# Kernel tuning notes

Hardware: AMD Instinct MI355X
Metric: run time of the kernel (lower is better)

The kernel has to match this reference:

```python
import jax, jax.numpy as jnp
import numpy as np
from jax import lax

# program token ids
PAD, START, END, SCENE, INTERSECT, FILT, RELATE, QUERY = range(8)
SKIP = (PAD, START, END)


def conv2d(x, w, b, dil=1):
    # 'same' padding for odd kernels (3x3 pad=dil, 1x1 pad=0), NCHW/OIHW
    pad = dil * (w.shape[2] // 2)
    y = lax.conv_general_dilated(x, w, (1, 1), [(pad, pad), (pad, pad)],
                                 rhs_dilation=(dil, dil),
                                 dimension_numbers=('NCHW', 'OIHW', 'NCHW'))
    return y + b[None, :, None, None]


def maxpool2(x):
    return lax.reduce_window(x, -jnp.inf, lax.max, (1, 1, 2, 2), (1, 1, 2, 2), 'VALID')


def exec_program(prog, feat_input, p):
    """Run one (concrete) program over a batch of stem features. prog: tuple of ints,
    executed in reversed order exactly like TbDNet.forward."""
    B, _, H, W = feat_input.shape
    output = feat_input
    saved = None
    for t in reversed(prog):
        if t in SKIP:
            continue
        if t == SCENE:
            saved = output
            output = jnp.ones((B, 1, H, W), feat_input.dtype)
        elif t == INTERSECT:  # AndModule: elementwise min of attentions
            output = jnp.minimum(output, saved)
        elif t == FILT:
            a = feat_input * output  # [B,D,H,W] * [B,1,H,W]
            a = jax.nn.relu(conv2d(a, p['att_w1'], p['att_b1']))
            a = jax.nn.relu(conv2d(a, p['att_w2'], p['att_b2']))
            output = jax.nn.sigmoid(conv2d(a, p['att_w3'], p['att_b3']))
        elif t == RELATE:  # RelateModule: dilated conv stack (1,2,4,8,1) -> conv1x1 sigmoid
            a = feat_input * output
            for w, b, d in ((p['rel_w1'], p['rel_b1'], 1), (p['rel_w2'], p['rel_b2'], 2),
                            (p['rel_w3'], p['rel_b3'], 4), (p['rel_w4'], p['rel_b4'], 8),
                            (p['rel_w5'], p['rel_b5'], 1)):
                a = jax.nn.relu(conv2d(a, w, b, d))
            output = jax.nn.sigmoid(conv2d(a, p['rel_w6'], p['rel_b6']))
        elif t == QUERY:
            a = feat_input * output
            a = jax.nn.relu(conv2d(a, p['qry_w1'], p['qry_b1']))
            output = jax.nn.relu(conv2d(a, p['qry_w2'], p['qry_b2']))
    return output


def tbd_forward(feats, programs_np, p):
    B = feats.shape[0]
    stem = jax.nn.relu(conv2d(feats, p['stem_w1'], p['stem_b1']))
    stem = jax.nn.relu(conv2d(stem, p['stem_w2'], p['stem_b2']))  # [B,D,H,W]
    D, H, W = stem.shape[1], stem.shape[2], stem.shape[3]
    # group samples by identical program so dispatch runs batched, not per-sample
    groups = {}
    for n in range(B):
        groups.setdefault(tuple(int(v) for v in programs_np[n]), []).append(n)
    mod_out = jnp.zeros((B, D, H, W), feats.dtype)
    for prog, idxs in groups.items():
        idx = jnp.array(idxs)
        mod_out = mod_out.at[idx].set(exec_program(prog, stem[idx], p))
    # classifier: conv1x1 -> relu -> maxpool2 -> flatten -> fc -> relu -> fc
    x = jax.nn.relu(conv2d(mod_out, p['cls_w'], p['cls_b']))
    x = maxpool2(x)                        # [B,1024,7,7]
    x = x.reshape(B, -1)                   # [B,50176]
    x = jax.nn.relu(x @ p['fc1_w'].T + p['fc1_b'])
    return x @ p['fc2_w'].T + p['fc2_b']   # [B,28]


def setup_inputs() -> dict:
    key = jax.random.key(0)
    ks = iter(jax.random.split(key, 64))
    def rn(shape, s=0.05):
        return jax.random.normal(next(ks), shape, dtype=jnp.float32) * s
    B, Cin, H, W, D, P, L, A = 64, 1024, 14, 14, 128, 1024, 1024, 28
    feats = jax.random.normal(next(ks), (B, Cin, H, W), dtype=jnp.float32)
    # stored programs; execution order is reversed(stored)
    progA = [START, QUERY, FILT, RELATE, FILT, SCENE, END, PAD]            # scene->filter->relate->filter->query
    progB = [START, QUERY, INTERSECT, FILT, SCENE, FILT, SCENE, END]       # two filter branches -> intersect -> query
    programs = jnp.array([progA] * (B // 2) + [progB] * (B // 2), dtype=jnp.int32)
    inp = {'feats': feats, 'programs': programs,
           'stem_w1': rn((D, Cin, 3, 3), 0.02), 'stem_b1': rn((D,)),
           'stem_w2': rn((D, D, 3, 3)), 'stem_b2': rn((D,)),
           'att_w1': rn((D, D, 3, 3)), 'att_b1': rn((D,)),
           'att_w2': rn((D, D, 3, 3)), 'att_b2': rn((D,)),
           'att_w3': rn((1, D, 1, 1)), 'att_b3': rn((1,)),
           'rel_w1': rn((D, D, 3, 3)), 'rel_b1': rn((D,)),
           'rel_w2': rn((D, D, 3, 3)), 'rel_b2': rn((D,)),
           'rel_w3': rn((D, D, 3, 3)), 'rel_b3': rn((D,)),
           'rel_w4': rn((D, D, 3, 3)), 'rel_b4': rn((D,)),
           'rel_w5': rn((D, D, 3, 3)), 'rel_b5': rn((D,)),
           'rel_w6': rn((1, D, 1, 1)), 'rel_b6': rn((1,)),
           'qry_w1': rn((D, D, 3, 3)), 'qry_b1': rn((D,)),
           'qry_w2': rn((D, D, 3, 3)), 'qry_b2': rn((D,)),
           'cls_w': rn((P, D, 1, 1)), 'cls_b': rn((P,)),
           'fc1_w': rn((L, P * (H // 2) * (W // 2)), 0.01), 'fc1_b': rn((L,)),
           'fc2_w': rn((A, L)), 'fc2_b': rn((A,))}
    return inp


PARAM_NAMES = ['stem_w1', 'stem_b1', 'stem_w2', 'stem_b2',
               'att_w1', 'att_b1', 'att_w2', 'att_b2', 'att_w3', 'att_b3',
               'rel_w1', 'rel_b1', 'rel_w2', 'rel_b2', 'rel_w3', 'rel_b3',
               'rel_w4', 'rel_b4', 'rel_w5', 'rel_b5', 'rel_w6', 'rel_b6',
               'qry_w1', 'qry_b1', 'qry_w2', 'qry_b2',
               'cls_w', 'cls_b', 'fc1_w', 'fc1_b', 'fc2_w', 'fc2_b']


def reference(feats, programs, stem_w1, stem_b1, stem_w2, stem_b2,
              att_w1, att_b1, att_w2, att_b2, att_w3, att_b3,
              rel_w1, rel_b1, rel_w2, rel_b2, rel_w3, rel_b3,
              rel_w4, rel_b4, rel_w5, rel_b5, rel_w6, rel_b6,
              qry_w1, qry_b1, qry_w2, qry_b2,
              cls_w, cls_b, fc1_w, fc1_b, fc2_w, fc2_b):
    vals = [stem_w1, stem_b1, stem_w2, stem_b2,
            att_w1, att_b1, att_w2, att_b2, att_w3, att_b3,
            rel_w1, rel_b1, rel_w2, rel_b2, rel_w3, rel_b3,
            rel_w4, rel_b4, rel_w5, rel_b5, rel_w6, rel_b6,
            qry_w1, qry_b1, qry_w2, qry_b2,
            cls_w, cls_b, fc1_w, fc1_b, fc2_w, fc2_b]
    p = dict(zip(PARAM_NAMES, vals))
    return tbd_forward(feats, np.asarray(programs), p)
```

## Files before the change

### kernel.cpp

```cpp
#include <hip/hip_runtime.h>
#include <math.h>


typedef __attribute__((ext_vector_type(8)))  short   short8;
typedef __attribute__((ext_vector_type(8)))  __bf16  bf16x8;
typedef __attribute__((ext_vector_type(4)))  float   f32x4;

#define NROUNDS 12
#define NKS 98

#define B_WSTEM1 0UL
#define B_WSTEM2 2359296UL
#define B_WMOD   2654208UL
#define B_WCLS   5308416UL
#define B_STEM   5570560UL
#define B_XA     8781824UL
#define B_XB     11993088UL
#define B_FEAT   15204352UL
#define B_ATTN   18415616UL
#define B_SAVED  18465792UL
#define B_SCHED  18515968UL
#define B_ACTB   18520064UL
#define B_FC1T   24942592UL
#define B_P1X1   25204736UL
#define B_S1P    67108864UL
#define B_FC1P   100663296UL

__device__ __forceinline__ unsigned short f2bf(float f) {
    unsigned int b = __float_as_uint(f);
    b += 0x7fffu + ((b >> 16) & 1u);
    return (unsigned short)(b >> 16);
}
__device__ __forceinline__ float bf2f(unsigned short u) {
    return __uint_as_float(((unsigned int)u) << 16);
}
__device__ __forceinline__ f32x4 mfma16(bf16x8 a, bf16x8 b, f32x4 c) {
    return __builtin_amdgcn_mfma_f32_16x16x32_bf16(a, b, c, 0, 0, 0);
}

struct RepackArgs { const float* src[12]; };

__global__ __launch_bounds__(256) void k_repack(RepackArgs a, char* ws)
{
    const int y = blockIdx.y;
    const float* __restrict__ src = a.src[y];
    int gid = blockIdx.x * 256 + threadIdx.x;
    int gsz = gridDim.x * 256;
    if (y == 11) {
        unsigned short* dst = (unsigned short*)(ws + B_WCLS);
        for (int i = gid; i < 131072; i += gsz) dst[i] = f2bf(src[i]);
    } else {
        const int IC = (y == 0) ? 1024 : 128;
        const int lg = (y == 0) ? 10 : 7;
        unsigned short* dst = (unsigned short*)(ws + ((y == 0) ? B_WSTEM1
                                    : (y == 1) ? B_WSTEM2
                                    : B_WMOD + (size_t)(y - 2) * 294912));
        const int total = 9 << (lg + 7);
        for (int i = gid; i < total; i += gsz) {
            int ic = i & (IC - 1);
            int oc = (i >> lg) & 127;
            int t  = i >> (lg + 7);
            dst[i] = f2bf(src[((size_t)oc * IC + ic) * 9 + t]);
        }
    }
}

__global__ __launch_bounds__(256) void k_decode_init(const int* __restrict__ prog, char* ws)
{
    int gid = blockIdx.x * 256 + threadIdx.x;
    int gsz = gridDim.x * 256;
    float* attn  = (float*)(ws + B_ATTN);
    float* saved = (float*)(ws + B_SAVED);
    float* p1    = (float*)(ws + B_P1X1);
    for (int i = gid; i < 64 * 196; i += gsz) { attn[i] = 1.0f; saved[i] = 1.0f; }
    for (int i = gid; i < 8 * 64 * 196; i += gsz) p1[i] = 0.0f;
    unsigned int* fz = (unsigned int*)(ws + B_FEAT);
    for (int i = gid; i < 64 * 25088 / 2; i += gsz) fz[i] = 0u;
    if (gid < 64) {
        int n = gid;
        int ent[NROUNDS];
        for (int r = 0; r < NROUNDS; ++r) ent[r] = 0;
        int rc = 0, nslot = 0;
        int pscene = 0, pinter = 0, pmat = 0, pmw = 0;
#define PREBITS ((pscene<<17)|(pinter<<18)|(pmat<<19)|(pmw<<22))
#define CLRPRE  (pscene = pinter = pmat = pmw = 0)
#define EMIT(v) do { if (rc < NROUNDS) ent[rc++] = (v); } while (0)
        for (int j = 7; j >= 0; --j) {
            int t = prog[n * 8 + j];
            switch (t) {
                case 3: pscene = 1; break;
                case 4: pinter = 1; break;
                case 5: {
                    int e1 = 3 | (0<<4) | (1<<8) | (1<<12) | (2<<13) | (0<<15) | PREBITS;
                    CLRPRE; EMIT(e1);
                    int e2 = 3 | (1<<4) | (1<<8) | (0<<12) | (0<<13) | (1<<15)
                               | (1<<23) | (0<<24) | (nslot<<25);
                    EMIT(e2);
                    pmat = nslot + 1; pmw = 0; nslot++;
                    break;
                }
                case 6: {
                    int e1 = 3 | (2<<4) | (1<<8) | (1<<12) | (2<<13) | (0<<15) | PREBITS;
                    CLRPRE; EMIT(e1);
                    EMIT(3 | (3<<4) | (2<<8) | (0<<12) | (0<<13) | (1<<15));
                    EMIT(3 | (4<<4) | (4<<8) | (0<<12) | (1<<13) | (0<<15));
                    EMIT(3 | (5<<4) | (8<<8) | (0<<12) | (0<<13) | (1<<15));
                    EMIT(3 | (6<<4) | (1<<8) | (0<<12) | (1<<13) | (0<<15)
                           | (1<<23) | (1<<24) | (nslot<<25));
                    pmat = nslot + 1; pmw = 1; nslot++;
                    break;
                }
                case 7: {
                    int e1 = 3 | (7<<4) | (1<<8) | (1<<12) | (2<<13) | (0<<15) | PREBITS;
                    CLRPRE; EMIT(e1);
                    EMIT(3 | (8<<4) | (1<<8) | (0<<12) | (0<<13) | (2<<15));
                    break;
                }
                default: break;
            }
        }
#undef EMIT
#undef PREBITS
#undef CLRPRE
        int* sched = (int*)(ws + B_SCHED);
        for (int r = 0; r < NROUNDS; ++r) sched[n * NROUNDS + r] = ent[r];
    }
}

__global__ __launch_bounds__(512) void k_stem1p(const float* __restrict__ feats,
                                                const unsigned short* __restrict__ wrep,
                                                char* ws)
{
    __shared__ unsigned short s_img[197 * 136];
    const int bx = blockIdx.x;
    const int n = bx >> 3, ks = bx & 7;
    const int tid = threadIdx.x, lane = tid & 63;
    const int w = tid >> 6, wm = w & 1, wn = w >> 1;
    const int l15 = lane & 15, lq = lane >> 4;

    if (tid < 68) ((unsigned int*)s_img)[196 * 68 + tid] = 0u;

    int pglob[4], pbyt[4], pyv[4], pxv[4];
#pragma unroll
    for (int j = 0; j < 4; ++j) {
        int p  = (wn + 4 * j) * 16 + l15;
        pglob[j] = p;
        int py = p / 14;
        pyv[j] = (p < 196) ? py : 10000;
        pxv[j] = p - py * 14;
        pbyt[j] = p * 272 + lq * 16;
    }
    const int zaddr = 196 * 272 + lq * 16;
    const int nJ = (wn == 0) ? 4 : 3;

    f32x4 acc[4][4];
#pragma unroll
    for (int m = 0; m < 4; ++m)
#pragma unroll
        for (int j = 0; j < 4; ++j) acc[m][j] = (f32x4){0.f, 0.f, 0.f, 0.f};

    const int icg = tid & 31;
    const int qq0 = tid >> 5;
    const int icb = ks * 128;

    const float* sf = feats + ((size_t)n * 1024 + icb) * 196;
    for (int qq = qq0; qq < 49; qq += 16) {
        const float* p0 = sf + icg * 4 * 196 + qq * 4;
        float4 r0 = *(const float4*)(p0);
        float4 r1 = *(const float4*)(p0 + 196);
        float4 r2 = *(const float4*)(p0 + 392);
        float4 r3 = *(const float4*)(p0 + 588);
#pragma unroll
        for (int e = 0; e < 4; ++e) {
            uint2 v;
            v.x = (unsigned int)f2bf(((const float*)&r0)[e]) |
                  ((unsigned int)f2bf(((const float*)&r1)[e]) << 16);
            v.y = (unsigned int)f2bf(((const float*)&r2)[e]) |
                  ((unsigned int)f2bf(((const float*)&r3)[e]) << 16);
            *(uint2*)(s_img + (qq * 4 + e) * 136 + icg * 4) = v;
        }
    }
    __syncthreads();

#pragma unroll
    for (int t = 0; t < 9; ++t) {
        const int dy = t / 3 - 1, dx = t % 3 - 1;
        int baddr[4];
#pragma unroll
        for (int j = 0; j < 4; ++j) {
            int yy = pyv[j] + dy, xx = pxv[j] + dx;
            bool ok = ((unsigned)yy < 14u) && ((unsigned)xx < 14u);
            baddr[j] = ok ? (pbyt[j] + (dy * 14 + dx) * 272) : zaddr;
        }
#pragma unroll
        for (int kc = 0; kc < 4; ++kc) {
            const unsigned short* wt = wrep +
                ((size_t)(t * 128 + wm * 64 + l15) * 1024 + icb + kc * 32 + lq * 8);
            bf16x8 am[4];
#pragma unroll
            for (int m = 0; m < 4; ++m)
                am[m] = *(const bf16x8*)(wt + (size_t)m * 16 * 1024);
#pragma unroll
            for (int j = 0; j < 4; ++j) {
                if (j < nJ) {
                    bf16x8 b = *(const bf16x8*)((const char*)s_img + baddr[j] + kc * 64);
#pragma unroll
                    for (int m = 0; m < 4; ++m)
                        acc[m][j] = mfma16(am[m], b, acc[m][j]);
                }
            }
        }
    }

    unsigned short* part = (unsigned short*)(ws + B_S1P);
#pragma unroll
    for (int m = 0; m < 4; ++m) {
        const int oc = wm * 64 + m * 16 + lq * 4;
#pragma unroll
        for (int j = 0; j < 4; ++j) {
            if (j < nJ) {
                int p = pglob[j];
                if (p < 196) {
                    unsigned int lo = (unsigned int)f2bf(acc[m][j][0]) |
                                      ((unsigned int)f2bf(acc[m][j][1]) << 16);
                    unsigned int hi = (unsigned int)f2bf(acc[m][j][2]) |
                                      ((unsigned int)f2bf(acc[m][j][3]) << 16);
                    uint2 pk; pk.x = lo; pk.y = hi;
                    *(uint2*)(part + (((size_t)ks * 64 + n) * 196 + p) * 128 + oc) = pk;
                }
            }
        }
    }
}

__global__ __launch_bounds__(256) void k_stem1r(const char* __restrict__ ws_c,
                                                const float* __restrict__ bias,
                                                unsigned short* __restrict__ xa)
{
    int i = blockIdx.x * 256 + threadIdx.x;
    const unsigned short* part = (const unsigned short*)(ws_c + B_S1P);
    int oc8 = (i & 15) * 8;
    int np  = i >> 4;
    float s[8] = {};
#pragma unroll
    for (int ks = 0; ks < 8; ++ks) {
        short8 v = *(const short8*)(part + (((size_t)ks * 64) * 196 + np) * 128 + oc8);
#pragma unroll
        for (int e = 0; e < 8; ++e) s[e] += bf2f((unsigned short)v[e]);
    }
    short8 o;
#pragma unroll
    for (int e = 0; e < 8; ++e)
        o[e] = (short)f2bf(fmaxf(s[e] + bias[oc8 + e], 0.f));
    *(short8*)(xa + (size_t)np * 128 + oc8) = o;
}

__device__ void conv_core32(const unsigned short* __restrict__ srcB,
                            const float* __restrict__ s_gate,
                            const unsigned short* __restrict__ wrep,
                            const float* __restrict__ bias,
                            unsigned short* __restrict__ dst,
                            int dil, int oct, int pxh,
                            unsigned short* s_img,
                            int post, const float* __restrict__ pwv,
                            float* __restrict__ pdst)
{
    const int tid  = threadIdx.x, lane = tid & 63;
    const int w    = tid >> 6, wm = w & 1, wn = w >> 1;
    const int l15  = lane & 15, lq = lane >> 4;

    if (tid < 68) ((unsigned int*)s_img)[196 * 68 + tid] = 0u;

    int pglob[4], pbyt[4], pyv[4], pxv[4];
#pragma unroll
    for (int j = 0; j < 4; ++j) {
        int nt = wn + 2 * j;
        int p  = (pxh * 7 + nt) * 16 + l15;
        pglob[j] = p;
        int py = p / 14;
        pyv[j] = (p < 196) ? py : 10000;
        pxv[j] = p - py * 14;
        pbyt[j] = p * 272 + lq * 16;
    }
    const int zaddr = 196 * 272 + lq * 16;
    const int nNT = (wn == 0) ? 4 : 3;

    f32x4 acc[4];
#pragma unroll
    for (int j = 0; j < 4; ++j) acc[j] = (f32x4){0.f, 0.f, 0.f, 0.f};

    if (s_gate) {
        for (int i = tid; i < 196 * 16; i += 256) {
            int p = i >> 4, c8 = (i & 15) * 8;
            short8 v = *(const short8*)(srcB + p * 128 + c8);
            float g = s_gate[p];
            short8 ov;
#pragma unroll
            for (int e = 0; e < 8; ++e)
                ov[e] = (short)f2bf(bf2f((unsigned short)v[e]) * g);
            *(short8*)(s_img + p * 136 + c8) = ov;
        }
    } else {
        for (int i = tid; i < 196 * 16; i += 256) {
            int p = i >> 4, c8 = (i & 15) * 8;
            *(short8*)(s_img + p * 136 + c8) = *(const short8*)(srcB + p * 128 + c8);
        }
    }
    __syncthreads();

    const unsigned short* wlane = wrep + (size_t)(oct * 32 + wm * 16 + l15) * 128 + lq * 8;
#pragma unroll
    for (int t = 0; t < 9; ++t) {
        const int dy = (t / 3 - 1) * dil, dx = (t % 3 - 1) * dil;
        int baddr[4];
#pragma unroll
        for (int j = 0; j < 4; ++j) {
            int yy = pyv[j] + dy, xx = pxv[j] + dx;
            bool ok = ((unsigned)yy < 14u) && ((unsigned)xx < 14u);
            baddr[j] = ok ? (pbyt[j] + (dy * 14 + dx) * 272) : zaddr;
        }
        const unsigned short* wt = wlane + (size_t)(t * 128) * 128;
#pragma unroll
        for (int kc = 0; kc < 4; ++kc) {
            bf16x8 a0 = *(const bf16x8*)(wt + kc * 32);
#pragma unroll
            for (int j = 0; j < 4; ++j) {
                if (j < nNT) {
                    bf16x8 b = *(const bf16x8*)((const char*)s_img + baddr[j] + kc * 64);
                    acc[j] = mfma16(a0, b, acc[j]);
                }
            }
        }
    }

    const int oc = oct * 32 + wm * 16 + lq * 4;
    const float4 b4 = *(const float4*)(bias + oc);
    float4 wv4;
    if (post) wv4 = *(const float4*)(pwv + oc);
#pragma unroll
    for (int j = 0; j < 4; ++j) {
        if (j < nNT) {
            int p = pglob[j];
            if (p < 196) {
                float v0 = fmaxf(acc[j][0] + b4.x, 0.f);
                float v1 = fmaxf(acc[j][1] + b4.y, 0.f);
                float v2 = fmaxf(acc[j][2] + b4.z, 0.f);
                float v3 = fmaxf(acc[j][3] + b4.w, 0.f);
                uint2 pk;
                pk.x = (unsigned int)f2bf(v0) | ((unsigned int)f2bf(v1) << 16);
                pk.y = (unsigned int)f2bf(v2) | ((unsigned int)f2bf(v3) << 16);
                *(uint2*)(dst + p * 128 + oc) = pk;
                if (post) {
                    float s = v0 * wv4.x + v1 * wv4.y + v2 * wv4.z + v3 * wv4.w;
                    atomicAdd(pdst + p, s);
                }
            }
        }
    }
}

__global__ __launch_bounds__(256) void k_conv_stem2(const unsigned short* __restrict__ srcBall,
                                                    const unsigned short* __restrict__ wrep,
                                                    const float* __restrict__ bias,
                                                    unsigned short* __restrict__ dstall)
{
    __shared__ unsigned short s_img[197 * 136];
    const int n = blockIdx.x >> 3, oct = (blockIdx.x >> 1) & 3, pxh = blockIdx.x & 1;
    conv_core32(srcBall + (size_t)n * 25088, nullptr, wrep, bias,
                dstall + (size_t)n * 25088, 1, oct, pxh, s_img, 0, nullptr, nullptr);
}

struct RArgs {
    char* ws;
    const float* mbias[9];
    const float* w1x1[2];
    const float* b1x1[2];
};

__global__ __launch_bounds__(256) void k_round(RArgs a, int r)
{
    __shared__ unsigned short s_img[197 * 136];
    __shared__ float s_gate[196];
    const int bx = blockIdx.x;
    const int n = bx >> 3, oct = (bx >> 1) & 3, pxh = bx & 1;
    char* ws = a.ws;
    const int* sched = (const int*)(ws + B_SCHED);
    const int e = sched[n * NROUNDS + r];
    if ((e & 15) == 0) return;
    const int tid = threadIdx.x;
    const int wset = (e >> 4) & 15, dil = (e >> 8) & 15, gatef = (e >> 12) & 1;
    const int srcid = (e >> 13) & 3, dstid = (e >> 15) & 3;
    const int fscene = (e >> 17) & 1, finter = (e >> 18) & 1;
    const int mslot = (e >> 19) & 7, mw = (e >> 22) & 1;
    const int post = (e >> 23) & 1, pw = (e >> 24) & 1, pslot = (e >> 25) & 7;

    float* attn  = (float*)(ws + B_ATTN)  + n * 196;
    float* saved = (float*)(ws + B_SAVED) + n * 196;
    float* p1    = (float*)(ws + B_P1X1);

    if (gatef) {
        if (tid < 196) {
            float cur = attn[tid];
            if (mslot) {
                float pv = p1[(size_t)(mslot - 1) * 12544 + n * 196 + tid];
                cur = 1.0f / (1.0f + __expf(-(pv + a.b1x1[mw][0])));
            }
            if (fscene) { saved[tid] = cur; cur = 1.0f; }
            if (finter) { cur = fminf(cur, saved[tid]); }
            if (mslot | fscene | finter) attn[tid] = cur;
            s_gate[tid] = cur;
        }
        __syncthreads();
    }

    const unsigned short* src = (const unsigned short*)(ws +
            (srcid == 2 ? B_STEM : srcid == 1 ? B_XB : B_XA)) + (size_t)n * 25088;
    unsigned short* dst = (unsigned short*)(ws +
            (dstid == 2 ? B_FEAT : dstid == 1 ? B_XB : B_XA)) + (size_t)n * 25088;
    const unsigned short* wrep = (const unsigned short*)(ws + B_WMOD) + (size_t)wset * 9 * 128 * 128;

    conv_core32(src, gatef ? s_gate : nullptr, wrep, a.mbias[wset], dst,
                dil, oct, pxh, s_img,
                post, post ? a.w1x1[pw] : nullptr,
                post ? (p1 + (size_t)pslot * 12544 + n * 196) : nullptr);
}

__global__ __launch_bounds__(256) void k_cls_pool(const unsigned short* __restrict__ featall,
                                                  const unsigned short* __restrict__ clsw,
                                                  const float* __restrict__ clsb,
                                                  unsigned short* __restrict__ actB)
{
    __shared__ char smem[197 * 272 + 64 * 200 * 4];
    unsigned short* s_img = (unsigned short*)smem;
    float* s_pool = (float*)(smem + 197 * 272);
    const int n = blockIdx.x >> 4, pt = blockIdx.x & 15;
    const int tid = threadIdx.x, lane = tid & 63, w = tid >> 6;
    const int l15 = lane & 15, lq = lane >> 4;
    const unsigned short* feat = featall + (size_t)n * 25088;

    if (tid < 68) ((unsigned int*)s_img)[196 * 68 + tid] = 0u;
    for (int i = tid; i < 196 * 16; i += 256) {
        int p = i >> 4, c8 = (i & 15) * 8;
        *(short8*)(s_img + p * 136 + c8) = *(const short8*)(feat + p * 128 + c8);
    }
    f32x4 acc[14];
#pragma unroll
    for (int j = 0; j < 14; ++j) acc[j] = (f32x4){0.f, 0.f, 0.f, 0.f};
    __syncthreads();

    const unsigned short* wl = clsw + (size_t)(pt * 64 + w * 16 + l15) * 128 + lq * 8;
#pragma unroll
    for (int kc = 0; kc < 4; ++kc) {
        bf16x8 a0 = *(const bf16x8*)(wl + kc * 32);
#pragma unroll
        for (int j = 0; j < 14; ++j) {
            int p = j * 16 + l15;
            int ba = (p < 196) ? (p * 272 + lq * 16 + kc * 64) : (196 * 272 + lq * 16);
            bf16x8 b = *(const bf16x8*)((const char*)s_img + ba);
            acc[j] = mfma16(a0, b, acc[j]);
        }
    }
    const int oc = pt * 64 + w * 16 + lq * 4;
    const float4 b4 = *(const float4*)(clsb + oc);
    const int pl = w * 16 + lq * 4;
#pragma unroll
    for (int j = 0; j < 14; ++j) {
        int p = j * 16 + l15;
        if (p < 196) {
            s_pool[(pl + 0) * 200 + p] = fmaxf(acc[j][0] + b4.x, 0.f);
            s_pool[(pl + 1) * 200 + p] = fmaxf(acc[j][1] + b4.y, 0.f);
            s_pool[(pl + 2) * 200 + p] = fmaxf(acc[j][2] + b4.z, 0.f);
            s_pool[(pl + 3) * 200 + p] = fmaxf(acc[j][3] + b4.w, 0.f);
        }
    }
    __syncthreads();
    for (int i = tid; i < 64 * 49; i += 256) {
        int plx = i / 49, q = i - plx * 49;
        int py = q / 7, qx = q - py * 7;
        const float* rp = s_pool + plx * 200 + py * 28 + qx * 2;
        float m = fmaxf(fmaxf(rp[0], rp[1]), fmaxf(rp[14], rp[15]));
        int k = (pt * 64 + plx) * 49 + q;
        int kb = k >> 6, lq2 = (k >> 4) & 3, hi = (k >> 3) & 1, e = k & 7;
        actB[((((size_t)kb * 4 + lq2) * 2 + hi) * 64 + n) * 8 + e] = f2bf(m);
    }
}

__global__ __launch_bounds__(256) void k_fc1p(const unsigned short* __restrict__ actB,
                                              const float* __restrict__ w,
                                              float* __restrict__ part)
{
    __shared__ unsigned short s_w[64 * 264];
    const int jt = blockIdx.x & 15, ks = blockIdx.x >> 4;
    const int tid = threadIdx.x, lane = tid & 63, wv = tid >> 6;
    const int l15 = lane & 15, lq = lane >> 4;
    const int k0 = ks * 512;
    const int r4 = tid & 3, l4 = (tid >> 2) & 15, rw = tid >> 6;

    f32x4 acc[4];
#pragma unroll
    for (int t = 0; t < 4; ++t) acc[t] = (f32x4){0.f, 0.f, 0.f, 0.f};

    float4 pf[4][4];

#define FC1_LOAD(ss_) do {                                                        \
    _Pragma("unroll")                                                             \
    for (int pass = 0; pass < 4; ++pass) {                                        \
        const int row_ = pass * 16 + rw * 4 + r4;                                 \
        const float* wp_ = w + (size_t)(jt * 64 + row_) * 50176 + k0              \
                             + (ss_) * 256 + l4 * 16;                             \
        pf[pass][0] = *(const float4*)(wp_);                                      \
        pf[pass][1] = *(const float4*)(wp_ + 4);                                  \
        pf[pass][2] = *(const float4*)(wp_ + 8);                                  \
        pf[pass][3] = *(const float4*)(wp_ + 12);                                 \
    } } while (0)

    FC1_LOAD(0);

    for (int ss = 0; ss < 2; ++ss) {
        __syncthreads();
#pragma unroll
        for (int pass = 0; pass < 4; ++pass) {
            const int row = pass * 16 + rw * 4 + r4;
            bf16x8 c0, c1;
            c0[0] = (__bf16)pf[pass][0].x; c0[1] = (__bf16)pf[pass][0].y;
            c0[2] = (__bf16)pf[pass][0].z; c0[3] = (__bf16)pf[pass][0].w;
            c0[4] = (__bf16)pf[pass][1].x; c0[5] = (__bf16)pf[pass][1].y;
            c0[6] = (__bf16)pf[pass][1].z; c0[7] = (__bf16)pf[pass][1].w;
            c1[0] = (__bf16)pf[pass][2].x; c1[1] = (__bf16)pf[pass][2].y;
            c1[2] = (__bf16)pf[pass][2].z; c1[3] = (__bf16)pf[pass][2].w;
            c1[4] = (__bf16)pf[pass][3].x; c1[5] = (__bf16)pf[pass][3].y;
            c1[6] = (__bf16)pf[pass][3].z; c1[7] = (__bf16)pf[pass][3].w;
            *(bf16x8*)(s_w + row * 264 + l4 * 16)     = c0;
            *(bf16x8*)(s_w + row * 264 + l4 * 16 + 8) = c1;
        }
        __syncthreads();
        if (ss < 1) FC1_LOAD(1);

        const unsigned short* arow = s_w + (wv * 16 + l15) * 264;
#pragma unroll
        for (int kk = 0; kk < 8; ++kk) {
            bf16x8 a = *(const bf16x8*)(arow + kk * 32 + lq * 8);
            const int kglob = k0 + ss * 256 + kk * 32 + lq * 8;
            const int kb = kglob >> 6, lq2 = (kglob >> 4) & 3, hi = (kglob >> 3) & 1;
            const unsigned short* bp = actB +
                ((((size_t)kb * 4 + lq2) * 2 + hi) * 64 + l15) * 8;
#pragma unroll
            for (int t = 0; t < 4; ++t) {
                bf16x8 b = *(const bf16x8*)(bp + t * 128);
                acc[t] = mfma16(a, b, acc[t]);
            }
        }
    }
#undef FC1_LOAD

    float* pbase = part + ((size_t)ks * 1024 + jt * 64 + wv * 16 + lq * 4) * 64 + l15;
#pragma unroll
    for (int t = 0; t < 4; ++t)
#pragma unroll
        for (int r = 0; r < 4; ++r)
            pbase[(size_t)r * 64 + t * 16] = acc[t][r];
}

__global__ __launch_bounds__(256) void k_fc1r(const float* __restrict__ part,
                                              const float* __restrict__ b,
                                              float* __restrict__ fc1T)
{
    int i = blockIdx.x * 256 + threadIdx.x;
    if (i >= 65536) return;
    float s = 0.0f;
    for (int ks = 0; ks < NKS; ++ks) s += part[(size_t)ks * 65536 + i];
    int j = i >> 6;
    fc1T[i] = fmaxf(s + b[j], 0.0f);
}

__global__ __launch_bounds__(256) void k_fc2(const float* __restrict__ fc1T,
                                             const float* __restrict__ w,
                                             const float* __restrict__ b,
                                             float* __restrict__ out)
{
    __shared__ float red[256];
    const int a_ = blockIdx.x;
    const int tid = threadIdx.x, lane = tid & 63, q = tid >> 6;
    float acc = 0.0f;
    const float* wr = w + (size_t)a_ * 1024;
    for (int k = q * 256; k < q * 256 + 256; ++k)
        acc = fmaf(fc1T[k * 64 + lane], wr[k], acc);
    red[tid] = acc;
    __syncthreads();
    if (q == 0) {
        float s = red[tid] + red[tid + 64] + red[tid + 128] + red[tid + 192] + b[a_];
        out[lane * 28 + a_] = s;
    }
}

extern "C" void kernel_launch(void* const* d_in, const int* in_sizes, int n_in,
                              void* d_out, int out_size, void* d_ws, size_t ws_size,
                              hipStream_t stream)
{
    const float* feats = (const float*)d_in[0];
    const int*   prog  = (const int*)d_in[1];
    char* ws  = (char*)d_ws;
    float* out = (float*)d_out;

    RepackArgs ra;
    ra.src[0]  = (const float*)d_in[2];
    ra.src[1]  = (const float*)d_in[4];
    ra.src[2]  = (const float*)d_in[6];
    ra.src[3]  = (const float*)d_in[8];
    ra.src[4]  = (const float*)d_in[12];
    ra.src[5]  = (const float*)d_in[14];
    ra.src[6]  = (const float*)d_in[16];
    ra.src[7]  = (const float*)d_in[18];
    ra.src[8]  = (const float*)d_in[20];
    ra.src[9]  = (const float*)d_in[24];
    ra.src[10] = (const float*)d_in[26];
    ra.src[11] = (const float*)d_in[28];

    k_repack<<<dim3(64, 12), 256, 0, stream>>>(ra, ws);
    k_decode_init<<<256, 256, 0, stream>>>(prog, ws);

    k_stem1p<<<512, 512, 0, stream>>>(feats, (const unsigned short*)(ws + B_WSTEM1), ws);
    k_stem1r<<<784, 256, 0, stream>>>(ws, (const float*)d_in[3],
                                      (unsigned short*)(ws + B_XA));

    k_conv_stem2<<<512, 256, 0, stream>>>((const unsigned short*)(ws + B_XA),
                                          (const unsigned short*)(ws + B_WSTEM2),
                                          (const float*)d_in[5],
                                          (unsigned short*)(ws + B_STEM));

    RArgs ga;
    ga.ws = ws;
    ga.mbias[0] = (const float*)d_in[7];
    ga.mbias[1] = (const float*)d_in[9];
    ga.mbias[2] = (const float*)d_in[13];
    ga.mbias[3] = (const float*)d_in[15];
    ga.mbias[4] = (const float*)d_in[17];
    ga.mbias[5] = (const float*)d_in[19];
    ga.mbias[6] = (const float*)d_in[21];
    ga.mbias[7] = (const float*)d_in[25];
    ga.mbias[8] = (const float*)d_in[27];
    ga.w1x1[0]  = (const float*)d_in[10];
    ga.w1x1[1]  = (const float*)d_in[22];
    ga.b1x1[0]  = (const float*)d_in[11];
    ga.b1x1[1]  = (const float*)d_in[23];

    for (int r = 0; r < NROUNDS; ++r)
        k_round<<<512, 256, 0, stream>>>(ga, r);

    k_cls_pool<<<1024, 256, 0, stream>>>((const unsigned short*)(ws + B_FEAT),
                                         (const unsigned short*)(ws + B_WCLS),
                                         (const float*)d_in[29],
                                         (unsigned short*)(ws + B_ACTB));
    k_fc1p<<<1568, 256, 0, stream>>>((const unsigned short*)(ws + B_ACTB),
                                     (const float*)d_in[30], (float*)(ws + B_FC1P));
    k_fc1r<<<256, 256, 0, stream>>>((const float*)(ws + B_FC1P), (const float*)d_in[31],
                                    (float*)(ws + B_FC1T));
    k_fc2<<<28, 256, 0, stream>>>((const float*)(ws + B_FC1T), (const float*)d_in[32],
                                  (const float*)d_in[33], out);
}
```

Baseline: 525.9 us.

## Fuse round launches into a persistent cooperative kernel with grid syncs

Merges the stem reduce, stem conv2 and every program round into one cooperative persistent kernel of 256 blocks by 512 threads, with grid.sync between stages. Each block now handles a full image and output-channel tile instead of half the pixels. The repack and decode/init kernels are folded into one launch, and fc1-reduce plus fc2 become a single cooperative kernel. The goal is to remove many launch gaps and the per-round schedule decode overhead, at the cost of grid-wide barriers, half the block count and larger blocks. NROUNDS drops from 12 to 11, which shrinks the schedule.

Result: slower. 785.6 us (+49.4%).

```diff
diff --git a/kernel.cpp b/kernel.cpp
--- a/kernel.cpp
+++ b/kernel.cpp
@@ -1,12 +1,15 @@
 #include <hip/hip_runtime.h>
+#include <hip/hip_cooperative_groups.h>
 #include <math.h>
+
+namespace cg = cooperative_groups;
 
 
 typedef __attribute__((ext_vector_type(8)))  short   short8;
 typedef __attribute__((ext_vector_type(8)))  __bf16  bf16x8;
 typedef __attribute__((ext_vector_type(4)))  float   f32x4;
 
-#define NROUNDS 12
+#define NROUNDS 11
 #define NKS 98
 
 #define B_WSTEM1 0UL
@@ -38,37 +41,38 @@
     return __builtin_amdgcn_mfma_f32_16x16x32_bf16(a, b, c, 0, 0, 0);
 }
 
-struct RepackArgs { const float* src[12]; };
-
-__global__ __launch_bounds__(256) void k_repack(RepackArgs a, char* ws)
-{
-    const int y = blockIdx.y;
-    const float* __restrict__ src = a.src[y];
-    int gid = blockIdx.x * 256 + threadIdx.x;
-    int gsz = gridDim.x * 256;
-    if (y == 11) {
-        unsigned short* dst = (unsigned short*)(ws + B_WCLS);
-        for (int i = gid; i < 131072; i += gsz) dst[i] = f2bf(src[i]);
-    } else {
-        const int IC = (y == 0) ? 1024 : 128;
-        const int lg = (y == 0) ? 10 : 7;
-        unsigned short* dst = (unsigned short*)(ws + ((y == 0) ? B_WSTEM1
-                                    : (y == 1) ? B_WSTEM2
-                                    : B_WMOD + (size_t)(y - 2) * 294912));
-        const int total = 9 << (lg + 7);
-        for (int i = gid; i < total; i += gsz) {
-            int ic = i & (IC - 1);
-            int oc = (i >> lg) & 127;
-            int t  = i >> (lg + 7);
-            dst[i] = f2bf(src[((size_t)oc * IC + ic) * 9 + t]);
-        }
-    }
-}
-
-__global__ __launch_bounds__(256) void k_decode_init(const int* __restrict__ prog, char* ws)
-{
-    int gid = blockIdx.x * 256 + threadIdx.x;
-    int gsz = gridDim.x * 256;
+struct PrepArgs { const float* src[12]; const int* prog; char* ws; };
+
+__global__ __launch_bounds__(256) void k_prep(PrepArgs a)
+{
+    char* ws = a.ws;
+    const int bx = blockIdx.x;
+    if (bx < 768) {
+        const int y = bx >> 6;
+        const float* __restrict__ src = a.src[y];
+        int gid = (bx & 63) * 256 + threadIdx.x;
+        int gsz = 64 * 256;
+        if (y == 11) {
+            unsigned short* dst = (unsigned short*)(ws + B_WCLS);
+            for (int i = gid; i < 131072; i += gsz) dst[i] = f2bf(src[i]);
+        } else {
+            const int IC = (y == 0) ? 1024 : 128;
+            const int lg = (y == 0) ? 10 : 7;
+            unsigned short* dst = (unsigned short*)(ws + ((y == 0) ? B_WSTEM1
+                                        : (y == 1) ? B_WSTEM2
+                                        : B_WMOD + (size_t)(y - 2) * 294912));
+            const int total = 9 << (lg + 7);
+            for (int i = gid; i < total; i += gsz) {
+                int ic = i & (IC - 1);
+                int oc = (i >> lg) & 127;
+                int t  = i >> (lg + 7);
+                dst[i] = f2bf(src[((size_t)oc * IC + ic) * 9 + t]);
+            }
+        }
+        return;
+    }
+    int gid = (bx - 768) * 256 + threadIdx.x;
+    int gsz = 256 * 256;
     float* attn  = (float*)(ws + B_ATTN);
     float* saved = (float*)(ws + B_SAVED);
     float* p1    = (float*)(ws + B_P1X1);
@@ -78,6 +82,7 @@
     for (int i = gid; i < 64 * 25088 / 2; i += gsz) fz[i] = 0u;
     if (gid < 64) {
         int n = gid;
+        const int* prog = a.prog;
         int ent[NROUNDS];
         for (int r = 0; r < NROUNDS; ++r) ent[r] = 0;
         int rc = 0, nslot = 0;
@@ -93,9 +98,8 @@
                 case 5: {
                     int e1 = 3 | (0<<4) | (1<<8) | (1<<12) | (2<<13) | (0<<15) | PREBITS;
                     CLRPRE; EMIT(e1);
-                    int e2 = 3 | (1<<4) | (1<<8) | (0<<12) | (0<<13) | (1<<15)
-                               | (1<<23) | (0<<24) | (nslot<<25);
-                    EMIT(e2);
+                    EMIT(3 | (1<<4) | (1<<8) | (0<<12) | (0<<13) | (1<<15)
+                           | (1<<23) | (0<<24) | (nslot<<25));
                     pmat = nslot + 1; pmw = 0; nslot++;
                     break;
                 }
@@ -233,49 +237,45 @@
     }
 }
 
-__global__ __launch_bounds__(256) void k_stem1r(const char* __restrict__ ws_c,
-                                                const float* __restrict__ bias,
-                                                unsigned short* __restrict__ xa)
-{
-    int i = blockIdx.x * 256 + threadIdx.x;
-    const unsigned short* part = (const unsigned short*)(ws_c + B_S1P);
-    int oc8 = (i & 15) * 8;
-    int np  = i >> 4;
-    float s[8] = {};
-#pragma unroll
-    for (int ks = 0; ks < 8; ++ks) {
-        short8 v = *(const short8*)(part + (((size_t)ks * 64) * 196 + np) * 128 + oc8);
-#pragma unroll
-        for (int e = 0; e < 8; ++e) s[e] += bf2f((unsigned short)v[e]);
-    }
-    short8 o;
-#pragma unroll
-    for (int e = 0; e < 8; ++e)
-        o[e] = (short)f2bf(fmaxf(s[e] + bias[oc8 + e], 0.f));
-    *(short8*)(xa + (size_t)np * 128 + oc8) = o;
-}
-
-__device__ void conv_core32(const unsigned short* __restrict__ srcB,
-                            const float* __restrict__ s_gate,
-                            const unsigned short* __restrict__ wrep,
-                            const float* __restrict__ bias,
-                            unsigned short* __restrict__ dst,
-                            int dil, int oct, int pxh,
-                            unsigned short* s_img,
-                            int post, const float* __restrict__ pwv,
-                            float* __restrict__ pdst)
-{
-    const int tid  = threadIdx.x, lane = tid & 63;
-    const int w    = tid >> 6, wm = w & 1, wn = w >> 1;
-    const int l15  = lane & 15, lq = lane >> 4;
+__device__ void conv512(const unsigned short* __restrict__ src,
+                        const float* __restrict__ s_gate,
+                        const unsigned short* __restrict__ wrep,
+                        const float* __restrict__ bias,
+                        unsigned short* __restrict__ dst,
+                        int dil, int oct,
+                        unsigned short* s_img,
+                        int post, const float* __restrict__ pwv,
+                        float* __restrict__ pdst)
+{
+    const int tid = threadIdx.x, lane = tid & 63;
+    const int w = tid >> 6, wm = w & 1, wn = w >> 1;
+    const int l15 = lane & 15, lq = lane >> 4;
 
     if (tid < 68) ((unsigned int*)s_img)[196 * 68 + tid] = 0u;
 
+    if (s_gate) {
+        for (int i = tid; i < 196 * 16; i += 512) {
+            int p = i >> 4, c8 = (i & 15) * 8;
+            short8 v = *(const short8*)(src + p * 128 + c8);
+            float g = s_gate[p];
+            short8 ov;
+#pragma unroll
+            for (int e = 0; e < 8; ++e)
+                ov[e] = (short)f2bf(bf2f((unsigned short)v[e]) * g);
+            *(short8*)(s_img + p * 136 + c8) = ov;
+        }
+    } else {
+        for (int i = tid; i < 196 * 16; i += 512) {
+            int p = i >> 4, c8 = (i & 15) * 8;
+            *(short8*)(s_img + p * 136 + c8) = *(const short8*)(src + p * 128 + c8);
+        }
+    }
+    __syncthreads();
+
     int pglob[4], pbyt[4], pyv[4], pxv[4];
 #pragma unroll
     for (int j = 0; j < 4; ++j) {
-        int nt = wn + 2 * j;
-        int p  = (pxh * 7 + nt) * 16 + l15;
+        int p  = (wn + 4 * j) * 16 + l15;
         pglob[j] = p;
         int py = p / 14;
         pyv[j] = (p < 196) ? py : 10000;
@@ -283,30 +283,11 @@
         pbyt[j] = p * 272 + lq * 16;
     }
     const int zaddr = 196 * 272 + lq * 16;
-    const int nNT = (wn == 0) ? 4 : 3;
+    const int nJ = (wn == 0) ? 4 : 3;
 
     f32x4 acc[4];
 #pragma unroll
     for (int j = 0; j < 4; ++j) acc[j] = (f32x4){0.f, 0.f, 0.f, 0.f};
-
-    if (s_gate) {
-        for (int i = tid; i < 196 * 16; i += 256) {
-            int p = i >> 4, c8 = (i & 15) * 8;
-            short8 v = *(const short8*)(srcB + p * 128 + c8);
-            float g = s_gate[p];
-            short8 ov;
-#pragma unroll
-            for (int e = 0; e < 8; ++e)
-                ov[e] = (short)f2bf(bf2f((unsigned short)v[e]) * g);
-            *(short8*)(s_img + p * 136 + c8) = ov;
-        }
-    } else {
-        for (int i = tid; i < 196 * 16; i += 256) {
-            int p = i >> 4, c8 = (i & 15) * 8;
-            *(short8*)(s_img + p * 136 + c8) = *(const short8*)(srcB + p * 128 + c8);
-        }
-    }
-    __syncthreads();
 
     const unsigned short* wlane = wrep + (size_t)(oct * 32 + wm * 16 + l15) * 128 + lq * 8;
 #pragma unroll
@@ -325,7 +306,7 @@
             bf16x8 a0 = *(const bf16x8*)(wt + kc * 32);
 #pragma unroll
             for (int j = 0; j < 4; ++j) {
-                if (j < nNT) {
+                if (j < nJ) {
                     bf16x8 b = *(const bf16x8*)((const char*)s_img + baddr[j] + kc * 64);
                     acc[j] = mfma16(a0, b, acc[j]);
                 }
@@ -339,7 +320,7 @@
     if (post) wv4 = *(const float4*)(pwv + oc);
 #pragma unroll
     for (int j = 0; j < 4; ++j) {
-        if (j < nNT) {
+        if (j < nJ) {
             int p = pglob[j];
             if (p < 196) {
                 float v0 = fmaxf(acc[j][0] + b4.x, 0.f);
@@ -359,70 +340,95 @@
     }
 }
 
-__global__ __launch_bounds__(256) void k_conv_stem2(const unsigned short* __restrict__ srcBall,
-                                                    const unsigned short* __restrict__ wrep,
-                                                    const float* __restrict__ bias,
-                                                    unsigned short* __restrict__ dstall)
-{
-    __shared__ unsigned short s_img[197 * 136];
-    const int n = blockIdx.x >> 3, oct = (blockIdx.x >> 1) & 3, pxh = blockIdx.x & 1;
-    conv_core32(srcBall + (size_t)n * 25088, nullptr, wrep, bias,
-                dstall + (size_t)n * 25088, 1, oct, pxh, s_img, 0, nullptr, nullptr);
-}
-
-struct RArgs {
+struct IArgs {
     char* ws;
+    const float* stem1b;
+    const float* stem2b;
     const float* mbias[9];
     const float* w1x1[2];
     const float* b1x1[2];
 };
 
-__global__ __launch_bounds__(256) void k_round(RArgs a, int r)
+__global__ __launch_bounds__(512) void k_interp(IArgs a)
 {
     __shared__ unsigned short s_img[197 * 136];
     __shared__ float s_gate[196];
+    cg::grid_group grid = cg::this_grid();
+    char* ws = a.ws;
     const int bx = blockIdx.x;
-    const int n = bx >> 3, oct = (bx >> 1) & 3, pxh = bx & 1;
-    char* ws = a.ws;
+    const int n = bx >> 2, oct = bx & 3;
+    const int tid = threadIdx.x;
+
+    {
+        const unsigned short* part = (const unsigned short*)(ws + B_S1P);
+        unsigned short* xa = (unsigned short*)(ws + B_XA);
+        for (int i = bx * 512 + tid; i < 64 * 196 * 16; i += 256 * 512) {
+            int oc8 = (i & 15) * 8;
+            int np  = i >> 4;
+            float s[8] = {};
+#pragma unroll
+            for (int ks = 0; ks < 8; ++ks) {
+                short8 v = *(const short8*)(part + (((size_t)ks * 64) * 196 + np) * 128 + oc8);
+#pragma unroll
+                for (int e = 0; e < 8; ++e) s[e] += bf2f((unsigned short)v[e]);
+            }
+            short8 o;
+#pragma unroll
+            for (int e = 0; e < 8; ++e)
+                o[e] = (short)f2bf(fmaxf(s[e] + a.stem1b[oc8 + e], 0.f));
+            *(short8*)(xa + (size_t)np * 128 + oc8) = o;
+        }
+    }
+    grid.sync();
+
+    conv512((const unsigned short*)(ws + B_XA) + (size_t)n * 25088, nullptr,
+            (const unsigned short*)(ws + B_WSTEM2), a.stem2b,
+            (unsigned short*)(ws + B_STEM) + (size_t)n * 25088,
+            1, oct, s_img, 0, nullptr, nullptr);
+    grid.sync();
+
     const int* sched = (const int*)(ws + B_SCHED);
-    const int e = sched[n * NROUNDS + r];
-    if ((e & 15) == 0) return;
-    const int tid = threadIdx.x;
-    const int wset = (e >> 4) & 15, dil = (e >> 8) & 15, gatef = (e >> 12) & 1;
-    const int srcid = (e >> 13) & 3, dstid = (e >> 15) & 3;
-    const int fscene = (e >> 17) & 1, finter = (e >> 18) & 1;
-    const int mslot = (e >> 19) & 7, mw = (e >> 22) & 1;
-    const int post = (e >> 23) & 1, pw = (e >> 24) & 1, pslot = (e >> 25) & 7;
-
     float* attn  = (float*)(ws + B_ATTN)  + n * 196;
     float* saved = (float*)(ws + B_SAVED) + n * 196;
     float* p1    = (float*)(ws + B_P1X1);
 
-    if (gatef) {
-        if (tid < 196) {
-            float cur = attn[tid];
-            if (mslot) {
-                float pv = p1[(size_t)(mslot - 1) * 12544 + n * 196 + tid];
-                cur = 1.0f / (1.0f + __expf(-(pv + a.b1x1[mw][0])));
-            }
-            if (fscene) { saved[tid] = cur; cur = 1.0f; }
-            if (finter) { cur = fminf(cur, saved[tid]); }
-            if (mslot | fscene | finter) attn[tid] = cur;
-            s_gate[tid] = cur;
-        }
-        __syncthreads();
-    }
-
-    const unsigned short* src = (const unsigned short*)(ws +
-            (srcid == 2 ? B_STEM : srcid == 1 ? B_XB : B_XA)) + (size_t)n * 25088;
-    unsigned short* dst = (unsigned short*)(ws +
-            (dstid == 2 ? B_FEAT : dstid == 1 ? B_XB : B_XA)) + (size_t)n * 25088;
-    const unsigned short* wrep = (const unsigned short*)(ws + B_WMOD) + (size_t)wset * 9 * 128 * 128;
-
-    conv_core32(src, gatef ? s_gate : nullptr, wrep, a.mbias[wset], dst,
-                dil, oct, pxh, s_img,
-                post, post ? a.w1x1[pw] : nullptr,
-                post ? (p1 + (size_t)pslot * 12544 + n * 196) : nullptr);
+    for (int r = 0; r < NROUNDS; ++r) {
+        const int e = sched[n * NROUNDS + r];
+        if (e & 15) {
+            const int wset = (e >> 4) & 15, dil = (e >> 8) & 15, gatef = (e >> 12) & 1;
+            const int srcid = (e >> 13) & 3, dstid = (e >> 15) & 3;
+            const int fscene = (e >> 17) & 1, finter = (e >> 18) & 1;
+            const int mslot = (e >> 19) & 7, mw = (e >> 22) & 1;
+            const int post = (e >> 23) & 1, pw = (e >> 24) & 1, pslot = (e >> 25) & 7;
+
+            if (gatef) {
+                if (tid < 196) {
+                    float cur = attn[tid];
+                    if (mslot) {
+                        float pv = p1[(size_t)(mslot - 1) * 12544 + n * 196 + tid];
+                        cur = 1.0f / (1.0f + __expf(-(pv + a.b1x1[mw][0])));
+                    }
+                    if (fscene) { saved[tid] = cur; cur = 1.0f; }
+                    if (finter) { cur = fminf(cur, saved[tid]); }
+                    if (mslot | fscene | finter) attn[tid] = cur;
+                    s_gate[tid] = cur;
+                }
+                __syncthreads();
+            }
+
+            const unsigned short* src = (const unsigned short*)(ws +
+                    (srcid == 2 ? B_STEM : srcid == 1 ? B_XB : B_XA)) + (size_t)n * 25088;
+            unsigned short* dst = (unsigned short*)(ws +
+                    (dstid == 2 ? B_FEAT : dstid == 1 ? B_XB : B_XA)) + (size_t)n * 25088;
+            const unsigned short* wrep = (const unsigned short*)(ws + B_WMOD)
+                                         + (size_t)wset * 9 * 128 * 128;
+            conv512(src, gatef ? s_gate : nullptr, wrep, a.mbias[wset], dst,
+                    dil, oct, s_img,
+                    post, post ? a.w1x1[pw] : nullptr,
+                    post ? (p1 + (size_t)pslot * 12544 + n * 196) : nullptr);
+        }
+        grid.sync();
+    }
 }
 
 __global__ __launch_bounds__(256) void k_cls_pool(const unsigned short* __restrict__ featall,
@@ -561,35 +567,35 @@
             pbase[(size_t)r * 64 + t * 16] = acc[t][r];
 }
 
-__global__ __launch_bounds__(256) void k_fc1r(const float* __restrict__ part,
-                                              const float* __restrict__ b,
-                                              float* __restrict__ fc1T)
-{
-    int i = blockIdx.x * 256 + threadIdx.x;
-    if (i >= 65536) return;
-    float s = 0.0f;
-    for (int ks = 0; ks < NKS; ++ks) s += part[(size_t)ks * 65536 + i];
-    int j = i >> 6;
-    fc1T[i] = fmaxf(s + b[j], 0.0f);
-}
-
-__global__ __launch_bounds__(256) void k_fc2(const float* __restrict__ fc1T,
-                                             const float* __restrict__ w,
-                                             const float* __restrict__ b,
-                                             float* __restrict__ out)
-{
+__global__ __launch_bounds__(256) void k_fc1tail(const float* __restrict__ part,
+                                                 const float* __restrict__ b1,
+                                                 const float* __restrict__ w2,
+                                                 const float* __restrict__ b2,
+                                                 float* __restrict__ fc1T,
+                                                 float* __restrict__ out)
+{
+    cg::grid_group grid = cg::this_grid();
     __shared__ float red[256];
-    const int a_ = blockIdx.x;
-    const int tid = threadIdx.x, lane = tid & 63, q = tid >> 6;
-    float acc = 0.0f;
-    const float* wr = w + (size_t)a_ * 1024;
-    for (int k = q * 256; k < q * 256 + 256; ++k)
-        acc = fmaf(fc1T[k * 64 + lane], wr[k], acc);
-    red[tid] = acc;
-    __syncthreads();
-    if (q == 0) {
-        float s = red[tid] + red[tid + 64] + red[tid + 128] + red[tid + 192] + b[a_];
-        out[lane * 28 + a_] = s;
+    {
+        int i = blockIdx.x * 256 + threadIdx.x;
+        float s = 0.0f;
+        for (int ks = 0; ks < NKS; ++ks) s += part[(size_t)ks * 65536 + i];
+        fc1T[i] = fmaxf(s + b1[i >> 6], 0.0f);
+    }
+    grid.sync();
+    if (blockIdx.x < 28) {
+        const int a_ = blockIdx.x;
+        const int tid = threadIdx.x, lane = tid & 63, q = tid >> 6;
+        float acc = 0.0f;
+        const float* wr = w2 + (size_t)a_ * 1024;
+        for (int k = q * 256; k < q * 256 + 256; ++k)
+            acc = fmaf(fc1T[k * 64 + lane], wr[k], acc);
+        red[tid] = acc;
+        __syncthreads();
+        if (q == 0) {
+            float s = red[tid] + red[tid + 64] + red[tid + 128] + red[tid + 192] + b2[a_];
+            out[lane * 28 + a_] = s;
+        }
     }
 }
 
@@ -602,50 +608,45 @@
     char* ws  = (char*)d_ws;
     float* out = (float*)d_out;
 
-    RepackArgs ra;
-    ra.src[0]  = (const float*)d_in[2];
-    ra.src[1]  = (const float*)d_in[4];
-    ra.src[2]  = (const float*)d_in[6];
-    ra.src[3]  = (const float*)d_in[8];
-    ra.src[4]  = (const float*)d_in[12];
-    ra.src[5]  = (const float*)d_in[14];
-    ra.src[6]  = (const float*)d_in[16];
-    ra.src[7]  = (const float*)d_in[18];
-    ra.src[8]  = (const float*)d_in[20];
-    ra.src[9]  = (const float*)d_in[24];
-    ra.src[10] = (const float*)d_in[26];
-    ra.src[11] = (const float*)d_in[28];
-
-    k_repack<<<dim3(64, 12), 256, 0, stream>>>(ra, ws);
-    k_decode_init<<<256, 256, 0, stream>>>(prog, ws);
+    PrepArgs pa;
+    pa.src[0]  = (const float*)d_in[2];
+    pa.src[1]  = (const float*)d_in[4];
+    pa.src[2]  = (const float*)d_in[6];
+    pa.src[3]  = (const float*)d_in[8];
+    pa.src[4]  = (const float*)d_in[12];
+    pa.src[5]  = (const float*)d_in[14];
+    pa.src[6]  = (const float*)d_in[16];
+    pa.src[7]  = (const float*)d_in[18];
+    pa.src[8]  = (const float*)d_in[20];
+    pa.src[9]  = (const float*)d_in[24];
+    pa.src[10] = (const float*)d_in[26];
+    pa.src[11] = (const float*)d_in[28];
+    pa.prog = prog;
+    pa.ws = ws;
+    k_prep<<<1024, 256, 0, stream>>>(pa);
 
     k_stem1p<<<512, 512, 0, stream>>>(feats, (const unsigned short*)(ws + B_WSTEM1), ws);
-    k_stem1r<<<784, 256, 0, stream>>>(ws, (const float*)d_in[3],
-                                      (unsigned short*)(ws + B_XA));
-
-    k_conv_stem2<<<512, 256, 0, stream>>>((const unsigned short*)(ws + B_XA),
-                                          (const unsigned short*)(ws + B_WSTEM2),
-                                          (const float*)d_in[5],
-                                          (unsigned short*)(ws + B_STEM));
-
-    RArgs ga;
-    ga.ws = ws;
-    ga.mbias[0] = (const float*)d_in[7];
-    ga.mbias[1] = (const float*)d_in[9];
-    ga.mbias[2] = (const float*)d_in[13];
-    ga.mbias[3] = (const float*)d_in[15];
-    ga.mbias[4] = (const float*)d_in[17];
-    ga.mbias[5] = (const float*)d_in[19];
-    ga.mbias[6] = (const float*)d_in[21];
-    ga.mbias[7] = (const float*)d_in[25];
-    ga.mbias[8] = (const float*)d_in[27];
-    ga.w1x1[0]  = (const float*)d_in[10];
-    ga.w1x1[1]  = (const float*)d_in[22];
-    ga.b1x1[0]  = (const float*)d_in[11];
-    ga.b1x1[1]  = (const float*)d_in[23];
-
-    for (int r = 0; r < NROUNDS; ++r)
-        k_round<<<512, 256, 0, stream>>>(ga, r);
+
+    IArgs ia;
+    ia.ws = ws;
+    ia.stem1b = (const float*)d_in[3];
+    ia.stem2b = (const float*)d_in[5];
+    ia.mbias[0] = (const float*)d_in[7];
+    ia.mbias[1] = (const float*)d_in[9];
+    ia.mbias[2] = (const float*)d_in[13];
+    ia.mbias[3] = (const float*)d_in[15];
+    ia.mbias[4] = (const float*)d_in[17];
+    ia.mbias[5] = (const float*)d_in[19];
+    ia.mbias[6] = (const float*)d_in[21];
+    ia.mbias[7] = (const float*)d_in[25];
+    ia.mbias[8] = (const float*)d_in[27];
+    ia.w1x1[0]  = (const float*)d_in[10];
+    ia.w1x1[1]  = (const float*)d_in[22];
+    ia.b1x1[0]  = (const float*)d_in[11];
+    ia.b1x1[1]  = (const float*)d_in[23];
+    void* kp1[] = { (void*)&ia };
+    hipLaunchCooperativeKernel((const void*)k_interp, dim3(256), dim3(512),
+                               kp1, 0, stream);
 
     k_cls_pool<<<1024, 256, 0, stream>>>((const unsigned short*)(ws + B_FEAT),
                                          (const unsigned short*)(ws + B_WCLS),
@@ -653,8 +654,15 @@
                                          (unsigned short*)(ws + B_ACTB));
     k_fc1p<<<1568, 256, 0, stream>>>((const unsigned short*)(ws + B_ACTB),
                                      (const float*)d_in[30], (float*)(ws + B_FC1P));
-    k_fc1r<<<256, 256, 0, stream>>>((const float*)(ws + B_FC1P), (const float*)d_in[31],
-                                    (float*)(ws + B_FC1T));
-    k_fc2<<<28, 256, 0, stream>>>((const float*)(ws + B_FC1T), (const float*)d_in[32],
-                                  (const float*)d_in[33], out);
-}
+
+    const float* partp = (const float*)(ws + B_FC1P);
+    const float* b1p   = (const float*)d_in[31];
+    const float* w2p   = (const float*)d_in[32];
+    const float* b2p   = (const float*)d_in[33];
+    float* fc1Tp = (float*)(ws + B_FC1T);
+    float* outp  = out;
+    void* kp2[] = { (void*)&partp, (void*)&b1p, (void*)&w2p, (void*)&b2p,
+                    (void*)&fc1Tp, (void*)&outp };
+    hipLaunchCooperativeKernel((const void*)k_fc1tail, dim3(256), dim3(256),
+                               kp2, 0, stream);
+}
```
